# Kernel tuning notes

Hardware: AMD Instinct MI355X
Metric: run time of the kernel (lower is better)

The kernel has to match this reference:

```python
import jax, jax.numpy as jnp
import numpy as np


def setup_inputs() -> dict:
    key = jax.random.key(0)
    k1, k2, k3 = jax.random.split(key, 3)
    x = jax.random.normal(k1, (64, 64, 128, 128), dtype=jnp.float32)
    weight = jax.random.normal(k2, (256, 64, 3, 3), dtype=jnp.float32)
    bias = jax.random.normal(k3, (256,), dtype=jnp.float32)
    return {"x": x, "weight": weight, "bias": bias}


def reference(x, weight, bias):
    # Conv2d, stride 1, no padding (VALID), NCHW / OIHW layout
    y = jax.lax.conv_general_dilated(
        x, weight,
        window_strides=(1, 1),
        padding='VALID',
        dimension_numbers=('NCHW', 'OIHW', 'NCHW'),
    )
    y = y + bias[None, :, None, None]  # [B, C_out, H_out, W_out]
    # tanh-approximate GELU (matches the Triton kernel's formula)
    y = jax.nn.gelu(y, approximate=True)
    # global average pool over spatial dims -> [B, C_out]
    return jnp.mean(y, axis=(2, 3))
```

## Files before the change

kernel.cpp:

```cpp
#include <hip/hip_runtime.h>


typedef __attribute__((ext_vector_type(8))) short short8;
typedef __attribute__((ext_vector_type(4))) float floatx4;
typedef __attribute__((ext_vector_type(4))) unsigned int uintx4;
typedef __attribute__((ext_vector_type(2))) unsigned int uintx2;

#define HO 126
#define CIP 72

__device__ __forceinline__ unsigned int f2bf(float f) {
    unsigned int u = __float_as_uint(f);
    return (u + 0x7FFFu + ((u >> 16) & 1u)) >> 16;
}

__device__ __forceinline__ float gelu_t(float y) {
    float p = __builtin_fmaf(0.044715f, y * y, 1.0f);
    float z2 = -2.3022084f * y * p;
    float e = exp2f(z2);
    return y * __builtin_amdgcn_rcpf(1.0f + e);
}

__global__ __launch_bounds__(256)
void prep_kernel(const float* __restrict__ wgt, float* __restrict__ out,
                 unsigned short* __restrict__ wb2) {
    int g = blockIdx.x * 256 + threadIdx.x;
    if (g < 64 * 256) out[g] = 0.f;
    if (g < 147456) {
        int j    = g & 7;
        int lane = (g >> 3) & 63;
        int fc   = g >> 9;
        int cog  = fc & 15;
        int half = (fc >> 4) & 1;
        int tap  = fc >> 5;
        int li = lane & 15, quad = lane >> 4;
        int co = cog * 16 + li;
        int ci = half * 32 + quad * 8 + j;
        wb2[g] = (unsigned short)f2bf(wgt[(co * 64 + ci) * 9 + tap]);
    }
}

__global__ __launch_bounds__(512, 4)
void conv_kernel(const float* __restrict__ x, const float* __restrict__ bias,
                 const unsigned short* __restrict__ wb2, float* __restrict__ out) {
    __shared__ unsigned short xs[3][130][CIP];

    const int bx = blockIdx.x;
    const int n = bx / HO;
    const int h = bx % HO;
    const int tid  = threadIdx.x;
    const int lane = tid & 63;
    const int wave = tid >> 6;
    const int li   = lane & 15;
    const int quad = lane >> 4;
    const int sc = wave & 3;
    const int sp = wave >> 2;
    const int coBase  = sc * 64;
    const int pixBase = sp * 64;

    {
        const int col = tid & 127;
        const int g   = tid >> 7;
        const float* xg = x + (size_t)n * 64 * 16384 + h * 128 + col;
#pragma unroll
        for (int i = 0; i < 12; ++i) {
            int idx = g * 12 + i;
            int r  = idx >> 4;
            int cq = idx & 15;
            float v0 = xg[(size_t)(cq * 4 + 0) * 16384 + r * 128];
            float v1 = xg[(size_t)(cq * 4 + 1) * 16384 + r * 128];
            float v2 = xg[(size_t)(cq * 4 + 2) * 16384 + r * 128];
            float v3 = xg[(size_t)(cq * 4 + 3) * 16384 + r * 128];
            uintx2 pk;
            pk.x = f2bf(v0) | (f2bf(v1) << 16);
            pk.y = f2bf(v2) | (f2bf(v3) << 16);
            *reinterpret_cast<uintx2*>(&xs[r][col][cq * 4]) = pk;
        }
    }

    floatx4 acc[16];
#pragma unroll
    for (int i = 0; i < 16; ++i) acc[i] = (floatx4){0.f, 0.f, 0.f, 0.f};

    __syncthreads();

    union Frag { uintx4 u; short8 s; };
    const unsigned short* xbase = &xs[0][pixBase + li][0] + quad * 8;
    const unsigned short* abase = wb2 + (size_t)(sc * 4) * 512 + lane * 8;

#pragma unroll
    for (int tap = 0; tap < 9; ++tap) {
        const int kh = tap / 3;
        const int kw = tap % 3;
        Frag a[8];
#pragma unroll
        for (int hf = 0; hf < 2; ++hf)
#pragma unroll
            for (int cf = 0; cf < 4; ++cf)
                a[hf * 4 + cf].u = *reinterpret_cast<const uintx4*>(
                    abase + (size_t)(((tap * 2 + hf) * 16) + cf) * 512);
#pragma unroll
        for (int hf = 0; hf < 2; ++hf)
#pragma unroll
            for (int pf = 0; pf < 4; ++pf) {
                Frag b;
                b.u = *reinterpret_cast<const uintx4*>(
                    xbase + (kh * 130 + kw + pf * 16) * CIP + hf * 32);
#pragma unroll
                for (int cf = 0; cf < 4; ++cf)
                    acc[cf * 4 + pf] = __builtin_amdgcn_mfma_f32_16x16x32_bf16(
                        a[hf * 4 + cf].s, b.s, acc[cf * 4 + pf], 0, 0, 0);
            }
    }

    const float inv = 1.0f / (126.f * 126.f);
#pragma unroll
    for (int cf = 0; cf < 4; ++cf) {
        const floatx4 bv = *reinterpret_cast<const floatx4*>(
            bias + coBase + cf * 16 + quad * 4);
        floatx4 s = (floatx4){0.f, 0.f, 0.f, 0.f};
#pragma unroll
        for (int pf = 0; pf < 4; ++pf) {
            bool valid = (pixBase + pf * 16 + li) < 126;
#pragma unroll
            for (int r = 0; r < 4; ++r) {
                float gv = gelu_t(acc[cf * 4 + pf][r] + bv[r]);
                s[r] += valid ? gv : 0.f;
            }
        }
#pragma unroll
        for (int r = 0; r < 4; ++r) {
            float v = s[r];
            v += __shfl_xor(v, 1);
            v += __shfl_xor(v, 2);
            v += __shfl_xor(v, 4);
            v += __shfl_xor(v, 8);
            if (li == 0)
                atomicAdd(&out[n * 256 + coBase + cf * 16 + quad * 4 + r], v * inv);
        }
    }
}

extern "C" void kernel_launch(void* const* d_in, const int* in_sizes, int n_in,
                              void* d_out, int out_size, void* d_ws, size_t ws_size,
                              hipStream_t stream) {
    const float* x    = (const float*)d_in[0];
    const float* wgt  = (const float*)d_in[1];
    const float* bias = (const float*)d_in[2];
    float* out = (float*)d_out;
    unsigned short* wb2 = (unsigned short*)d_ws;

    prep_kernel<<<576, 256, 0, stream>>>(wgt, out, wb2);
    conv_kernel<<<64 * HO, 512, 0, stream>>>(x, bias, wb2, out);
}
```

Baseline: 690.0 us.

## Switch conv MFMA to 32x32x16 bf16 tiles with register-prefetched fragments

Replaces the 16x16x32 MFMA tiling with 32x32x16 bf16 MFMAs. Each wave now computes 2x2 32x32 output blocks, and the prepacked weight layout and LDS fragment addressing change to match. The K loop is flattened into 36 steps, with A fragments triple-buffered and B fragments double-buffered in registers so that global and LDS loads for later steps overlap the current MFMAs. The epilogue is reworked for the 32-lane reduction. The intent is fewer MFMA issues and fewer fragment loads per FLOP; the risk is higher register pressure at the 512x4 launch bound and more shuffles and atomics in the epilogue.

```diff
diff --git a/kernel.cpp b/kernel.cpp
--- a/kernel.cpp
+++ b/kernel.cpp
@@ -3,6 +3,7 @@
 
 typedef __attribute__((ext_vector_type(8))) short short8;
 typedef __attribute__((ext_vector_type(4))) float floatx4;
+typedef __attribute__((ext_vector_type(16))) float floatx16;
 typedef __attribute__((ext_vector_type(4))) unsigned int uintx4;
 typedef __attribute__((ext_vector_type(2))) unsigned int uintx2;
 
@@ -29,16 +30,18 @@
     if (g < 147456) {
         int j    = g & 7;
         int lane = (g >> 3) & 63;
-        int fc   = g >> 9;
-        int cog  = fc & 15;
-        int half = (fc >> 4) & 1;
-        int tap  = fc >> 5;
-        int li = lane & 15, quad = lane >> 4;
-        int co = cog * 16 + li;
-        int ci = half * 32 + quad * 8 + j;
+        int f    = g >> 9;
+        int cog  = f & 7;
+        int ks   = (f >> 3) & 3;
+        int tap  = f >> 5;
+        int co = cog * 32 + (lane & 31);
+        int ci = ks * 16 + (lane >> 5) * 8 + j;
         wb2[g] = (unsigned short)f2bf(wgt[(co * 64 + ci) * 9 + tap]);
     }
 }
+
+#define AOFF(t, k, cf) ((size_t)((((t) * 4 + (k)) * 8 + (cf))) * 512)
+#define BOFF(t, k, pf) ((((t) / 3) * 130 + ((t) % 3) + (pf) * 32) * CIP + (k) * 16)
 
 __global__ __launch_bounds__(512, 4)
 void conv_kernel(const float* __restrict__ x, const float* __restrict__ bias,
@@ -51,8 +54,6 @@
     const int tid  = threadIdx.x;
     const int lane = tid & 63;
     const int wave = tid >> 6;
-    const int li   = lane & 15;
-    const int quad = lane >> 4;
     const int sc = wave & 3;
     const int sp = wave >> 2;
     const int coBase  = sc * 64;
@@ -62,7 +63,7 @@
         const int col = tid & 127;
         const int g   = tid >> 7;
         const float* xg = x + (size_t)n * 64 * 16384 + h * 128 + col;
-#pragma unroll
+#pragma unroll 12
         for (int i = 0; i < 12; ++i) {
             int idx = g * 12 + i;
             int r  = idx >> 4;
@@ -78,67 +79,81 @@
         }
     }
 
-    floatx4 acc[16];
+    floatx16 acc[2][2];
 #pragma unroll
-    for (int i = 0; i < 16; ++i) acc[i] = (floatx4){0.f, 0.f, 0.f, 0.f};
+    for (int cf = 0; cf < 2; ++cf)
+#pragma unroll
+        for (int pf = 0; pf < 2; ++pf)
+#pragma unroll
+            for (int r = 0; r < 16; ++r) acc[cf][pf][r] = 0.f;
 
     __syncthreads();
 
     union Frag { uintx4 u; short8 s; };
-    const unsigned short* xbase = &xs[0][pixBase + li][0] + quad * 8;
-    const unsigned short* abase = wb2 + (size_t)(sc * 4) * 512 + lane * 8;
+    const unsigned short* xb = &xs[0][pixBase + (lane & 31)][0] + (lane >> 5) * 8;
+    const unsigned short* ab = wb2 + (size_t)(sc * 2) * 512 + lane * 8;
 
+    Frag a[3][2];
+    Frag b[2][2];
 #pragma unroll
-    for (int tap = 0; tap < 9; ++tap) {
-        const int kh = tap / 3;
-        const int kw = tap % 3;
-        Frag a[8];
+    for (int cf = 0; cf < 2; ++cf) {
+        a[0][cf].u = *reinterpret_cast<const uintx4*>(ab + AOFF(0, 0, cf));
+        a[1][cf].u = *reinterpret_cast<const uintx4*>(ab + AOFF(0, 1, cf));
+    }
 #pragma unroll
-        for (int hf = 0; hf < 2; ++hf)
+    for (int pf = 0; pf < 2; ++pf)
+        b[0][pf].u = *reinterpret_cast<const uintx4*>(xb + BOFF(0, 0, pf));
+
+#pragma unroll 36
+    for (int u = 0; u < 36; ++u) {
+        if (u + 1 < 36) {
+            const int t1 = (u + 1) >> 2, k1 = (u + 1) & 3;
 #pragma unroll
-            for (int cf = 0; cf < 4; ++cf)
-                a[hf * 4 + cf].u = *reinterpret_cast<const uintx4*>(
-                    abase + (size_t)(((tap * 2 + hf) * 16) + cf) * 512);
+            for (int pf = 0; pf < 2; ++pf)
+                b[(u + 1) & 1][pf].u =
+                    *reinterpret_cast<const uintx4*>(xb + BOFF(t1, k1, pf));
+        }
+        if (u + 2 < 36) {
+            const int t2 = (u + 2) >> 2, k2 = (u + 2) & 3;
 #pragma unroll
-        for (int hf = 0; hf < 2; ++hf)
+            for (int cf = 0; cf < 2; ++cf)
+                a[(u + 2) % 3][cf].u =
+                    *reinterpret_cast<const uintx4*>(ab + AOFF(t2, k2, cf));
+        }
 #pragma unroll
-            for (int pf = 0; pf < 4; ++pf) {
-                Frag b;
-                b.u = *reinterpret_cast<const uintx4*>(
-                    xbase + (kh * 130 + kw + pf * 16) * CIP + hf * 32);
+        for (int cf = 0; cf < 2; ++cf)
 #pragma unroll
-                for (int cf = 0; cf < 4; ++cf)
-                    acc[cf * 4 + pf] = __builtin_amdgcn_mfma_f32_16x16x32_bf16(
-                        a[hf * 4 + cf].s, b.s, acc[cf * 4 + pf], 0, 0, 0);
-            }
+            for (int pf = 0; pf < 2; ++pf)
+                acc[cf][pf] = __builtin_amdgcn_mfma_f32_32x32x16_bf16(
+                    a[u % 3][cf].s, b[u & 1][pf].s, acc[cf][pf], 0, 0, 0);
     }
 
     const float inv = 1.0f / (126.f * 126.f);
+    const int colv = pixBase + (lane & 31);
+    const bool v0ok = colv < 126;
+    const bool v1ok = (colv + 32) < 126;
+    const int uhalf = lane >> 5;
 #pragma unroll
-    for (int cf = 0; cf < 4; ++cf) {
-        const floatx4 bv = *reinterpret_cast<const floatx4*>(
-            bias + coBase + cf * 16 + quad * 4);
-        floatx4 s = (floatx4){0.f, 0.f, 0.f, 0.f};
+    for (int cf = 0; cf < 2; ++cf)
 #pragma unroll
-        for (int pf = 0; pf < 4; ++pf) {
-            bool valid = (pixBase + pf * 16 + li) < 126;
+        for (int rg = 0; rg < 4; ++rg) {
+            const floatx4 bv = *reinterpret_cast<const floatx4*>(
+                bias + coBase + cf * 32 + rg * 8 + uhalf * 4);
 #pragma unroll
-            for (int r = 0; r < 4; ++r) {
-                float gv = gelu_t(acc[cf * 4 + pf][r] + bv[r]);
-                s[r] += valid ? gv : 0.f;
+            for (int jj = 0; jj < 4; ++jj) {
+                float g0 = gelu_t(acc[cf][0][rg * 4 + jj] + bv[jj]);
+                float g1 = gelu_t(acc[cf][1][rg * 4 + jj] + bv[jj]);
+                float v = (v0ok ? g0 : 0.f) + (v1ok ? g1 : 0.f);
+                v += __shfl_xor(v, 1);
+                v += __shfl_xor(v, 2);
+                v += __shfl_xor(v, 4);
+                v += __shfl_xor(v, 8);
+                v += __shfl_xor(v, 16);
+                if ((lane & 31) == 0)
+                    atomicAdd(&out[n * 256 + coBase + cf * 32 + rg * 8 + uhalf * 4 + jj],
+                              v * inv);
             }
         }
-#pragma unroll
-        for (int r = 0; r < 4; ++r) {
-            float v = s[r];
-            v += __shfl_xor(v, 1);
-            v += __shfl_xor(v, 2);
-            v += __shfl_xor(v, 4);
-            v += __shfl_xor(v, 8);
-            if (li == 0)
-                atomicAdd(&out[n * 256 + coBase + cf * 16 + quad * 4 + r], v * inv);
-        }
-    }
 }
 
 extern "C" void kernel_launch(void* const* d_in, const int* in_sizes, int n_in,
```

After: 875.0 us. 26.8% more time.
